# Kernel tuning notes

Measured on AMD Instinct MI355X. Metric: run time of the kernel, lower is better.

The kernel has to match this reference:

```python
import jax, jax.numpy as jnp
import numpy as np

D_MODEL = 1024
NUM_HEADS = 16
HEAD_DIM = D_MODEL // NUM_HEADS
BATCH = 4
SEQ = 2048


def setup_inputs() -> dict:
    key = jax.random.key(0)
    k_x, k_wqkv, k_bqkv, k_wo, k_bo = jax.random.split(key, 5)
    x = jax.random.normal(k_x, (BATCH, SEQ, D_MODEL), dtype=jnp.float32)
    # Linear params (flax Linear stores kernel as [in, out])
    s1 = 1.0 / np.sqrt(D_MODEL)
    W_qkv = jax.random.normal(k_wqkv, (D_MODEL, 3 * D_MODEL), dtype=jnp.float32) * s1
    b_qkv = jax.random.normal(k_bqkv, (3 * D_MODEL,), dtype=jnp.float32) * 0.01
    W_out = jax.random.normal(k_wo, (D_MODEL, D_MODEL), dtype=jnp.float32) * s1
    b_out = jax.random.normal(k_bo, (D_MODEL,), dtype=jnp.float32) * 0.01
    return {"x": x, "W_qkv": W_qkv, "b_qkv": b_qkv, "W_out": W_out, "b_out": b_out}


def reference(x, W_qkv, b_qkv, W_out, b_out):
    B, S, _ = x.shape
    qkv = x @ W_qkv + b_qkv                                   # [B,S,3D]
    qkv = qkv.reshape(B, S, 3, NUM_HEADS, HEAD_DIM)
    q, k, v = jnp.split(qkv, 3, axis=2)
    q = q.squeeze(2).transpose(0, 2, 1, 3)                    # [B,H,S,d]
    k = k.squeeze(2).transpose(0, 2, 1, 3)
    v = v.squeeze(2).transpose(0, 2, 1, 3)
    scores = jnp.einsum('bhqd,bhkd->bhqk', q, k) / jnp.sqrt(jnp.float32(HEAD_DIM))
    causal = jnp.tril(jnp.ones((S, S), dtype=bool))[None, None]
    scores = jnp.where(causal, scores, jnp.float32(-1e10))
    attn = jax.nn.softmax(scores, axis=-1)                    # [B,H,S,S]
    out = jnp.einsum('bhqk,bhkd->bhqd', attn, v)              # [B,H,S,d]
    out = out.transpose(0, 2, 1, 3).reshape(B, S, D_MODEL)
    return out @ W_out + b_out
```

## Files before the change

### kernel.cpp

```cpp
#include <hip/hip_runtime.h>

#define SEQ 2048
#define DM 1024
#define NH 16
#define HD 64
#define BATCH 4
#define M_TOK (BATCH * SEQ)

typedef _Float16 f16;
typedef _Float16 f16x8 __attribute__((ext_vector_type(8)));
typedef _Float16 f16x4 __attribute__((ext_vector_type(4)));
typedef float f32x4 __attribute__((ext_vector_type(4)));
typedef float f32x16 __attribute__((ext_vector_type(16)));

__device__ __forceinline__ f32x4 mfma16(f16x8 a, f16x8 b, f32x4 c) {
  return __builtin_amdgcn_mfma_f32_16x16x32_f16(a, b, c, 0, 0, 0);
}
__device__ __forceinline__ f32x16 mfma32(f16x8 a, f16x8 b, f32x16 c) {
  return __builtin_amdgcn_mfma_f32_32x32x16_f16(a, b, c, 0, 0, 0);
}

__device__ __forceinline__ void gload16(const void* g, void* l) {
  __builtin_amdgcn_global_load_lds((const __attribute__((address_space(1))) void*)g,
                                   (__attribute__((address_space(3))) void*)l, 16, 0, 0);
}

__global__ void cvt_f16_kernel(const float* __restrict__ in, f16* __restrict__ out, int n8) {
  int i = blockIdx.x * blockDim.x + threadIdx.x;
  if (i >= n8) return;
  float4 a = ((const float4*)in)[2 * i];
  float4 b = ((const float4*)in)[2 * i + 1];
  f16x8 v;
  v[0] = (f16)a.x; v[1] = (f16)a.y; v[2] = (f16)a.z; v[3] = (f16)a.w;
  v[4] = (f16)b.x; v[5] = (f16)b.y; v[6] = (f16)b.z; v[7] = (f16)b.w;
  *(f16x8*)(out + 8 * i) = v;
}

__global__ void transpose_cvt_kernel(const float* __restrict__ W, f16* __restrict__ Wt,
                                     int K, int N) {
  __shared__ float t[32][33];
  int tx = threadIdx.x & 31, ty = threadIdx.x >> 5;
  int c0 = blockIdx.x * 32, r0 = blockIdx.y * 32;
#pragma unroll
  for (int i = 0; i < 4; ++i)
    t[ty + 8 * i][tx] = W[(r0 + ty + 8 * i) * N + c0 + tx];
  __syncthreads();
#pragma unroll
  for (int i = 0; i < 4; ++i)
    Wt[(c0 + ty + 8 * i) * K + r0 + tx] = (f16)t[tx][ty + 8 * i];
}

template <typename OutT, bool SPLIT_V>
__global__ __launch_bounds__(256) void gemm_tn(const f16* __restrict__ A,
                                               const f16* __restrict__ Bt,
                                               const float* __restrict__ bias,
                                               OutT* __restrict__ C, f16* __restrict__ Vt,
                                               int M, int N, int K, int ldc) {
  __shared__ f16 Alds[128 * 64];
  __shared__ f16 Blds[128 * 64];
  const int tid = threadIdx.x;
  const int lane = tid & 63, wid = tid >> 6;
  const int l15 = lane & 15, l4 = lane >> 4;
  const int m0 = blockIdx.y * 128, n0 = blockIdx.x * 128;
  const int wr = wid >> 1, wc = wid & 1;

  f32x4 acc[4][4] = {};

  for (int k0 = 0; k0 < K; k0 += 64) {
    __syncthreads();
#pragma unroll
    for (int i = 0; i < 4; ++i) {
      int c = (wid * 4 + i) * 64 + lane;
      int row = c >> 3, cb = (c & 7) << 4;
      int sw = cb ^ ((row & 7) << 4);
      const char* gA = (const char*)(A + ((size_t)(m0 + row) * K + k0)) + sw;
      gload16(gA, (char*)Alds + ((wid * 4 + i) << 10));
      const char* gB = (const char*)(Bt + ((size_t)(n0 + row) * K + k0)) + sw;
      gload16(gB, (char*)Blds + ((wid * 4 + i) << 10));
    }
    asm volatile("s_waitcnt vmcnt(0)" ::: "memory");
    __syncthreads();

#pragma unroll
    for (int ks = 0; ks < 2; ++ks) {
      f16x8 af[4], bf[4];
      int cb = ((ks * 4 + l4) << 4);
#pragma unroll
      for (int mi = 0; mi < 4; ++mi) {
        int row = wr * 64 + mi * 16 + l15;
        af[mi] = *(const f16x8*)((const char*)Alds + row * 128 + (cb ^ ((row & 7) << 4)));
      }
#pragma unroll
      for (int ni = 0; ni < 4; ++ni) {
        int row = wc * 64 + ni * 16 + l15;
        bf[ni] = *(const f16x8*)((const char*)Blds + row * 128 + (cb ^ ((row & 7) << 4)));
      }
#pragma unroll
      for (int mi = 0; mi < 4; ++mi)
#pragma unroll
        for (int ni = 0; ni < 4; ++ni)
          acc[mi][ni] = mfma16(af[mi], bf[ni], acc[mi][ni]);
    }
  }

#pragma unroll
  for (int ni = 0; ni < 4; ++ni) {
    int col = n0 + wc * 64 + ni * 16 + l15;
    float bv = bias[col];
#pragma unroll
    for (int mi = 0; mi < 4; ++mi)
#pragma unroll
      for (int r = 0; r < 4; ++r) {
        int rowg = m0 + wr * 64 + mi * 16 + l4 * 4 + r;
        float val = acc[mi][ni][r] + bv;
        if (SPLIT_V && col >= 2 * DM) {
          int hdv = col - 2 * DM;
          int b = rowg >> 11, s = rowg & (SEQ - 1);
          Vt[(size_t)(b * 1024 + hdv) * SEQ + s] = (f16)val;
        } else {
          C[(size_t)rowg * ldc + col] = (OutT)val;
        }
      }
  }
}

union H2u { struct { f16 lo, hi; } s; unsigned u; };
union F8u { f16x8 v; unsigned u[4]; };

__global__ __launch_bounds__(256) void attn_kernel(const f16* __restrict__ qkh,
                                                   const f16* __restrict__ vtg,
                                                   f16* __restrict__ outp) {
  __shared__ f16 Klds[2][64 * 64];
  __shared__ f16 Vlds[2][64 * 64];
  const int tid = threadIdx.x;
  const int lane = tid & 63, wid = tid >> 6;
  const int lq = lane & 31, hi = lane >> 5;
  const int blk = blockIdx.x;
  const int xcd = blk & 7, sl = blk >> 3;
  const int bq = sl >> 4, qp = sl & 15;
  const int bh = xcd * 8 + bq;
  const int b = bh >> 4, h = bh & 15;
  const int hb = ((bq & 2) ? 15 : 0) ^ ((bq & 1) ? 3 : 0) ^ ((bq & 4) ? 5 : 0);
  const int q0 = (qp ^ hb) << 7;
  const int q0w = q0 + wid * 32;
  const int q_g = q0w + lq;

  const f16* qp_ptr = qkh + (size_t)(b * SEQ + q_g) * 2048 + h * HD;
  f16x8 qf[4];
#pragma unroll
  for (int s = 0; s < 4; ++s) {
    qf[s] = *(const f16x8*)(qp_ptr + s * 16 + hi * 8);
    qf[s] = qf[s] * (f16)0.125f;
  }

  const char* kbase = (const char*)qkh + ((size_t)(b * SEQ) * 2048 + 1024 + h * HD) * 2;
  const char* vbase = (const char*)vtg + ((size_t)(bh * 64) * SEQ) * 2;
  int srow[2], ssw[2], schunk[2];
#pragma unroll
  for (int i = 0; i < 2; ++i) {
    int c = (wid * 2 + i) * 64 + lane;
    srow[i] = c >> 3;
    ssw[i] = ((c & 7) << 4) ^ ((srow[i] & 7) << 4);
    schunk[i] = (wid * 2 + i) << 10;
  }

  f32x16 o0 = {}, o1 = {};
  float m_run = -3.0e38f, l_run = 0.f;
  const int ntile = (q0 >> 6) + 2;
  const int ntw = (q0w >> 6) + 1;
  const float L2E = 1.44269504f;

#pragma unroll
  for (int i = 0; i < 2; ++i) {
    gload16(kbase + (size_t)srow[i] * 4096 + ssw[i], (char*)Klds[0] + schunk[i]);
    gload16(vbase + (size_t)srow[i] * 4096 + ssw[i], (char*)Vlds[0] + schunk[i]);
  }
  __syncthreads();

  for (int t = 0; t < ntile; ++t) {
    const int cur = t & 1;
    const int kt = t << 6;
    if (t + 1 < ntile) {
      const int kn = kt + 64;
#pragma unroll
      for (int i = 0; i < 2; ++i) {
        gload16(kbase + (size_t)(kn + srow[i]) * 4096 + ssw[i], (char*)Klds[cur ^ 1] + schunk[i]);
        gload16(vbase + (size_t)srow[i] * 4096 + kn * 2 + ssw[i], (char*)Vlds[cur ^ 1] + schunk[i]);
      }
    }

    if (t < ntw) {
      f32x16 st0 = {}, st1 = {};
#pragma unroll
      for (int s = 0; s < 4; ++s) {
        int cb = ((2 * s + hi) << 4);
        f16x8 kf0 = *(const f16x8*)((const char*)Klds[cur] + lq * 128 + (cb ^ ((lq & 7) << 4)));
        f16x8 kf1 =
            *(const f16x8*)((const char*)Klds[cur] + (32 + lq) * 128 + (cb ^ ((lq & 7) << 4)));
        st0 = mfma32(kf0, qf[s], st0);
        st1 = mfma32(kf1, qf[s], st1);
      }
      if (t == ntw - 1) {
#pragma unroll
        for (int r = 0; r < 16; ++r) {
          int kl = (r & 3) + 8 * (r >> 2) + 4 * hi;
          if (kt + kl > q_g) st0[r] = -3.0e38f;
          if (kt + 32 + kl > q_g) st1[r] = -3.0e38f;
        }
      }
      float mx = st0[0];
#pragma unroll
      for (int r = 1; r < 16; ++r) mx = fmaxf(mx, st0[r]);
#pragma unroll
      for (int r = 0; r < 16; ++r) mx = fmaxf(mx, st1[r]);
      mx = fmaxf(mx, __shfl_xor(mx, 32));
      if (__any(mx > m_run)) {
        float mn = fmaxf(m_run, mx);
        float al = exp2f((m_run - mn) * L2E);
        m_run = mn;
        l_run *= al;
        o0 = o0 * al;
        o1 = o1 * al;
      }
      const float negmL = -m_run * L2E;
#pragma unroll
      for (int r = 0; r < 16; ++r) st0[r] = exp2f(fmaf(st0[r], L2E, negmL));
#pragma unroll
      for (int r = 0; r < 16; ++r) st1[r] = exp2f(fmaf(st1[r], L2E, negmL));
      float sm = st0[0];
#pragma unroll
      for (int r = 1; r < 16; ++r) sm += st0[r];
#pragma unroll
      for (int r = 0; r < 16; ++r) sm += st1[r];
      sm += __shfl_xor(sm, 32);
      l_run += sm;

#pragma unroll
      for (int s = 0; s < 4; ++s) {
        const f32x16& ps = (s < 2) ? st0 : st1;
        const int r0 = 8 * (s & 1);
        H2u a0, a1, a2, a3;
        a0.s.lo = (f16)ps[r0 + 0]; a0.s.hi = (f16)ps[r0 + 1];
        a1.s.lo = (f16)ps[r0 + 2]; a1.s.hi = (f16)ps[r0 + 3];
        a2.s.lo = (f16)ps[r0 + 4]; a2.s.hi = (f16)ps[r0 + 5];
        a3.s.lo = (f16)ps[r0 + 6]; a3.s.hi = (f16)ps[r0 + 7];
        unsigned ux = __shfl_xor(a0.u, 32), vx = __shfl_xor(a1.u, 32);
        unsigned wx = __shfl_xor(a2.u, 32), zx = __shfl_xor(a3.u, 32);
        F8u pb;
        pb.u[0] = hi ? wx : a0.u;
        pb.u[1] = hi ? zx : a1.u;
        pb.u[2] = hi ? a2.u : ux;
        pb.u[3] = hi ? a3.u : vx;
        int vb = ((2 * s + hi) << 4);
        f16x8 vf0 = *(const f16x8*)((const char*)Vlds[cur] + lq * 128 + (vb ^ ((lq & 7) << 4)));
        f16x8 vf1 =
            *(const f16x8*)((const char*)Vlds[cur] + (32 + lq) * 128 + (vb ^ ((lq & 7) << 4)));
        o0 = mfma32(vf0, pb.v, o0);
        o1 = mfma32(vf1, pb.v, o1);
      }
    }
    __syncthreads();
  }

  float rl = 1.0f / l_run;
  f16* outb = outp + (size_t)(b * SEQ + q_g) * DM + h * HD;
#pragma unroll
  for (int dvt = 0; dvt < 2; ++dvt) {
    const f32x16& ov = dvt ? o1 : o0;
#pragma unroll
    for (int rg = 0; rg < 4; ++rg) {
      f16x4 w4;
#pragma unroll
      for (int j = 0; j < 4; ++j) w4[j] = (f16)(ov[rg * 4 + j] * rl);
      *(f16x4*)(outb + dvt * 32 + 8 * rg + 4 * hi) = w4;
    }
  }
}

extern "C" void kernel_launch(void* const* d_in, const int* in_sizes, int n_in,
                              void* d_out, int out_size, void* d_ws, size_t ws_size,
                              hipStream_t stream) {
  const float* x = (const float*)d_in[0];
  const float* Wqkv = (const float*)d_in[1];
  const float* bqkv = (const float*)d_in[2];
  const float* Wout = (const float*)d_in[3];
  const float* bout = (const float*)d_in[4];
  float* out = (float*)d_out;

  char* ws = (char*)d_ws;
  f16* xh = (f16*)(ws);
  f16* qkh = (f16*)(ws + 16777216);
  f16* vt = (f16*)(ws + 16777216 + 33554432);
  f16* wqkvT = (f16*)(ws + 16777216 + 33554432 + 16777216);
  f16* woutT = (f16*)(ws + 16777216 + 33554432 + 16777216 + 6291456);
  f16* attno = xh;

  cvt_f16_kernel<<<(M_TOK * DM / 8 + 255) / 256, 256, 0, stream>>>(x, xh, M_TOK * DM / 8);
  transpose_cvt_kernel<<<dim3(3 * DM / 32, DM / 32), 256, 0, stream>>>(Wqkv, wqkvT, DM, 3 * DM);
  transpose_cvt_kernel<<<dim3(DM / 32, DM / 32), 256, 0, stream>>>(Wout, woutT, DM, DM);
  gemm_tn<f16, true><<<dim3(3 * DM / 128, M_TOK / 128), 256, 0, stream>>>(
      xh, wqkvT, bqkv, qkh, vt, M_TOK, 3 * DM, DM, 2048);
  attn_kernel<<<BATCH * NH * (SEQ / 128), 256, 0, stream>>>(qkh, vt, attno);
  gemm_tn<float, false><<<dim3(DM / 128, M_TOK / 128), 256, 0, stream>>>(
      attno, woutT, bout, out, nullptr, M_TOK, DM, DM, DM);
}
```

Baseline: 321.6 us.

## Pair causal query tiles per block for balanced attention work, lazy rescale

Each attention block now handles two 128-row query tiles, one from the end and one from the start of the sequence (p and 15-p), so every block does about the same amount of causal work. This halves the grid to 512 blocks and is meant to remove load imbalance and tail effects. It also adds a lazy online-softmax rescale that updates the running max only when the new max exceeds it by more than 8. That skips some rescale work but allows exp values up to about e^8, which could hurt f16 precision of the probabilities.

```diff
diff --git a/kernel.cpp b/kernel.cpp
--- a/kernel.cpp
+++ b/kernel.cpp
@@ -136,22 +136,11 @@
   const int lane = tid & 63, wid = tid >> 6;
   const int lq = lane & 31, hi = lane >> 5;
   const int blk = blockIdx.x;
-  const int xcd = blk & 7, sl = blk >> 3;
-  const int bq = sl >> 4, qp = sl & 15;
-  const int bh = xcd * 8 + bq;
+  const int xcd = blk & 7, rr = blk >> 3;
+  const int bh = xcd * 8 + (rr & 7);
+  const int p = rr >> 3;
   const int b = bh >> 4, h = bh & 15;
-  const int hb = ((bq & 2) ? 15 : 0) ^ ((bq & 1) ? 3 : 0) ^ ((bq & 4) ? 5 : 0);
-  const int q0 = (qp ^ hb) << 7;
-  const int q0w = q0 + wid * 32;
-  const int q_g = q0w + lq;
-
-  const f16* qp_ptr = qkh + (size_t)(b * SEQ + q_g) * 2048 + h * HD;
-  f16x8 qf[4];
-#pragma unroll
-  for (int s = 0; s < 4; ++s) {
-    qf[s] = *(const f16x8*)(qp_ptr + s * 16 + hi * 8);
-    qf[s] = qf[s] * (f16)0.125f;
-  }
+  const int qD = 15 - p, qS = p;
 
   const char* kbase = (const char*)qkh + ((size_t)(b * SEQ) * 2048 + 1024 + h * HD) * 2;
   const char* vbase = (const char*)vtg + ((size_t)(bh * 64) * SEQ) * 2;
@@ -164,11 +153,41 @@
     schunk[i] = (wid * 2 + i) << 10;
   }
 
+  int q0 = qD << 7;
+  int q_g = q0 + wid * 32 + lq;
+  int ntw = ((q0 + wid * 32) >> 6) + 1;
+  f16x8 qf[4];
   f32x16 o0 = {}, o1 = {};
   float m_run = -3.0e38f, l_run = 0.f;
-  const int ntile = (q0 >> 6) + 2;
-  const int ntw = (q0w >> 6) + 1;
   const float L2E = 1.44269504f;
+
+  auto load_q = [&]() {
+    const f16* qp_ptr = qkh + (size_t)(b * SEQ + q_g) * 2048 + h * HD;
+#pragma unroll
+    for (int s = 0; s < 4; ++s) {
+      qf[s] = *(const f16x8*)(qp_ptr + s * 16 + hi * 8);
+      qf[s] = qf[s] * (f16)0.125f;
+    }
+  };
+  auto store_out = [&]() {
+    float rl = 1.0f / l_run;
+    f16* outb = outp + (size_t)(b * SEQ + q_g) * DM + h * HD;
+#pragma unroll
+    for (int dvt = 0; dvt < 2; ++dvt) {
+      const f32x16& ov = dvt ? o1 : o0;
+#pragma unroll
+      for (int rg = 0; rg < 4; ++rg) {
+        f16x4 w4;
+#pragma unroll
+        for (int j = 0; j < 4; ++j) w4[j] = (f16)(ov[rg * 4 + j] * rl);
+        *(f16x4*)(outb + dvt * 32 + 8 * rg + 4 * hi) = w4;
+      }
+    }
+  };
+
+  load_q();
+  const int ntD = 2 * qD + 2;
+  const int ntT = ntD + 2 * qS + 2;
 
 #pragma unroll
   for (int i = 0; i < 2; ++i) {
@@ -177,19 +196,33 @@
   }
   __syncthreads();
 
-  for (int t = 0; t < ntile; ++t) {
+  for (int t = 0; t < ntT; ++t) {
     const int cur = t & 1;
-    const int kt = t << 6;
-    if (t + 1 < ntile) {
-      const int kn = kt + 64;
+    if (t + 1 < ntT) {
+      const int kn = (t + 1 < ntD) ? (t + 1) : (t + 1 - ntD);
 #pragma unroll
       for (int i = 0; i < 2; ++i) {
-        gload16(kbase + (size_t)(kn + srow[i]) * 4096 + ssw[i], (char*)Klds[cur ^ 1] + schunk[i]);
-        gload16(vbase + (size_t)srow[i] * 4096 + kn * 2 + ssw[i], (char*)Vlds[cur ^ 1] + schunk[i]);
-      }
-    }
-
-    if (t < ntw) {
+        gload16(kbase + (size_t)(kn * 64 + srow[i]) * 4096 + ssw[i],
+                (char*)Klds[cur ^ 1] + schunk[i]);
+        gload16(vbase + (size_t)srow[i] * 4096 + (size_t)kn * 128 + ssw[i],
+                (char*)Vlds[cur ^ 1] + schunk[i]);
+      }
+    }
+    if (t == ntD) {
+      store_out();
+#pragma unroll
+      for (int r2 = 0; r2 < 16; ++r2) { o0[r2] = 0.f; o1[r2] = 0.f; }
+      m_run = -3.0e38f;
+      l_run = 0.f;
+      q0 = qS << 7;
+      q_g = q0 + wid * 32 + lq;
+      ntw = ((q0 + wid * 32) >> 6) + 1;
+      load_q();
+    }
+    const int tt = (t >= ntD) ? (t - ntD) : t;
+
+    if (tt < ntw) {
+      const int kt = tt << 6;
       f32x16 st0 = {}, st1 = {};
 #pragma unroll
       for (int s = 0; s < 4; ++s) {
@@ -200,7 +233,7 @@
         st0 = mfma32(kf0, qf[s], st0);
         st1 = mfma32(kf1, qf[s], st1);
       }
-      if (t == ntw - 1) {
+      if (tt == ntw - 1) {
 #pragma unroll
         for (int r = 0; r < 16; ++r) {
           int kl = (r & 3) + 8 * (r >> 2) + 4 * hi;
@@ -214,7 +247,7 @@
 #pragma unroll
       for (int r = 0; r < 16; ++r) mx = fmaxf(mx, st1[r]);
       mx = fmaxf(mx, __shfl_xor(mx, 32));
-      if (__any(mx > m_run)) {
+      if (__any(mx - m_run > 8.0f)) {
         float mn = fmaxf(m_run, mx);
         float al = exp2f((m_run - mn) * L2E);
         m_run = mn;
@@ -262,19 +295,7 @@
     __syncthreads();
   }
 
-  float rl = 1.0f / l_run;
-  f16* outb = outp + (size_t)(b * SEQ + q_g) * DM + h * HD;
-#pragma unroll
-  for (int dvt = 0; dvt < 2; ++dvt) {
-    const f32x16& ov = dvt ? o1 : o0;
-#pragma unroll
-    for (int rg = 0; rg < 4; ++rg) {
-      f16x4 w4;
-#pragma unroll
-      for (int j = 0; j < 4; ++j) w4[j] = (f16)(ov[rg * 4 + j] * rl);
-      *(f16x4*)(outb + dvt * 32 + 8 * rg + 4 * hi) = w4;
-    }
-  }
+  store_out();
 }
 
 extern "C" void kernel_launch(void* const* d_in, const int* in_sizes, int n_in,
@@ -300,7 +321,7 @@
   transpose_cvt_kernel<<<dim3(DM / 32, DM / 32), 256, 0, stream>>>(Wout, woutT, DM, DM);
   gemm_tn<f16, true><<<dim3(3 * DM / 128, M_TOK / 128), 256, 0, stream>>>(
       xh, wqkvT, bqkv, qkh, vt, M_TOK, 3 * DM, DM, 2048);
-  attn_kernel<<<BATCH * NH * (SEQ / 128), 256, 0, stream>>>(qkh, vt, attno);
+  attn_kernel<<<512, 256, 0, stream>>>(qkh, vt, attno);
   gemm_tn<float, false><<<dim3(DM / 128, M_TOK / 128), 256, 0, stream>>>(
       attno, woutT, bout, out, nullptr, M_TOK, DM, DM, DM);
 }
```

Measured after the change: 300.7 us. 1.07x faster.
